# Optimization experiments

Measured on AMD Instinct MI355X. Metric: run time of the kernel, lower is better.

## Reference

```python
import jax, jax.numpy as jnp
import numpy as np

IN_DIM = 256
QK_DIM = IN_DIM // 8  # 32
B, H, W = 4, 64, 64


def setup_inputs() -> dict:
    key = jax.random.key(0)
    ks = jax.random.split(key, 8)
    s = 1.0 / np.sqrt(IN_DIM)
    return {
        "x": jax.random.normal(ks[0], (B, IN_DIM, H, W), dtype=jnp.float32),
        "Wq": jax.random.normal(ks[1], (QK_DIM, IN_DIM), dtype=jnp.float32) * s,
        "bq": jax.random.normal(ks[2], (QK_DIM,), dtype=jnp.float32) * 0.01,
        "Wk": jax.random.normal(ks[3], (QK_DIM, IN_DIM), dtype=jnp.float32) * s,
        "bk": jax.random.normal(ks[4], (QK_DIM,), dtype=jnp.float32) * 0.01,
        "Wv": jax.random.normal(ks[5], (IN_DIM, IN_DIM), dtype=jnp.float32) * s,
        "bv": jax.random.normal(ks[6], (IN_DIM,), dtype=jnp.float32) * 0.01,
        "gamma": jax.random.normal(ks[7], (1,), dtype=jnp.float32) * 0.1,
    }


def reference(x, Wq, bq, Wk, bk, Wv, bv, gamma):
    b, c, h, w = x.shape
    n = h * w
    xf = x.reshape(b, c, n)  # [b, c, n]
    # 1x1 convs are channel-wise linear maps over flattened spatial dim
    q = jnp.einsum('dc,bcn->bnd', Wq, xf) + bq  # [b, n, d]
    k = jnp.einsum('dc,bcn->bdn', Wk, xf) + bk[:, None]  # [b, d, n]
    attn = jax.nn.softmax(jnp.einsum('bnd,bdm->bnm', q, k), axis=-1)  # [b, n, n]
    v = jnp.einsum('ec,bcn->ben', Wv, xf) + bv[:, None]  # [b, c, n]
    # out[:, :, m] = sum_n v[:, :, n] * attn[m, n]  (bmm with attn^T)
    out = jnp.einsum('ben,bmn->bem', v, attn).reshape(b, c, h, w)
    return gamma * out + x
```

## Files before the change

### kernel.cpp

```cpp
#include <hip/hip_runtime.h>
#include <hip/hip_bf16.h>
#include <stdint.h>

#define DI __device__ __forceinline__

typedef float f32x4 __attribute__((ext_vector_type(4)));
typedef short bf16x8 __attribute__((ext_vector_type(8)));
typedef unsigned short u16x4 __attribute__((ext_vector_type(4)));

constexpr int BATCH = 4;
constexpr int C = 256;
constexpr int N = 4096;
constexpr int NO = 320;
constexpr int KB2 = 64;
constexpr int NT2 = N / KB2;

DI unsigned short f2bf(float f) {
  union { float f; unsigned int i; } v; v.f = f;
  unsigned int r = v.i + 0x7fffu + ((v.i >> 16) & 1u);
  return (unsigned short)(r >> 16);
}

__global__ __launch_bounds__(256) void prep_kernel(
    const float* __restrict__ Wq, const float* __restrict__ Wk, const float* __restrict__ Wv,
    const float* __restrict__ bq, const float* __restrict__ bk, const float* __restrict__ bv,
    unsigned short* __restrict__ Wcat, float* __restrict__ bcat) {
  int idx = blockIdx.x * 256 + threadIdx.x;
  if (idx < NO * C) {
    int row = idx >> 8, c = idx & 255;
    float v = (row < 32) ? Wq[row * 256 + c]
            : (row < 64) ? Wk[(row - 32) * 256 + c]
                         : Wv[(row - 64) * 256 + c];
    Wcat[idx] = f2bf(v);
  }
  if (idx < NO) {
    float v = (idx < 32) ? bq[idx] : (idx < 64) ? bk[idx - 32] : bv[idx - 64];
    bcat[idx] = v;
  }
}

__global__ __launch_bounds__(256) void proj_kernel(
    const float* __restrict__ x, const unsigned short* __restrict__ Wcat,
    const float* __restrict__ bcat,
    unsigned short* __restrict__ qarr, unsigned short* __restrict__ karr,
    unsigned short* __restrict__ vT) {
  __shared__ __align__(16) unsigned short ldsx[C][68];

  int b = blockIdx.y, n0 = blockIdx.x * 64;
  int t = threadIdx.x, lane = t & 63, w = t >> 6;
  int g = lane >> 4, cq = lane & 15;

  const float* xb = x + (size_t)b * C * N;
  {
    int csub = lane >> 4, m = lane & 15;
    #pragma unroll 4
    for (int cc = 0; cc < 16; ++cc) {
      int c = cc * 16 + w * 4 + csub;
      f32x4 v = *(const f32x4*)(xb + (size_t)c * N + n0 + m * 4);
      u16x4 h;
      h[0] = f2bf(v[0]); h[1] = f2bf(v[1]); h[2] = f2bf(v[2]); h[3] = f2bf(v[3]);
      *(u16x4*)(&ldsx[c][m * 4]) = h;
    }
  }
  __syncthreads();

  bf16x8 afrag[8];
  int nrow = w * 16 + cq;
  #pragma unroll
  for (int ks = 0; ks < 8; ++ks) {
    bf16x8 a;
    #pragma unroll
    for (int j = 0; j < 8; ++j) a[j] = (short)ldsx[ks * 32 + g * 8 + j][nrow];
    afrag[ks] = a;
  }
  __syncthreads();

  unsigned short (*vlds)[258] = (unsigned short (*)[258]) & ldsx[0][0];

  #pragma unroll 2
  for (int oc = 0; oc < 20; ++oc) {
    int o = oc * 16 + cq;
    f32x4 acc = {0.f, 0.f, 0.f, 0.f};
    const unsigned short* wrow = Wcat + o * 256;
    #pragma unroll
    for (int ks = 0; ks < 8; ++ks) {
      bf16x8 bf = *(const bf16x8*)(wrow + ks * 32 + g * 8);
      acc = __builtin_amdgcn_mfma_f32_16x16x32_bf16(afrag[ks], bf, acc, 0, 0, 0);
    }
    float bias = bcat[o];
    if (oc < 4) {
      unsigned short* dst = (oc < 2) ? qarr : karr;
      int od = ((oc & 1) << 4) + cq;
      #pragma unroll
      for (int r = 0; r < 4; ++r) {
        int n = n0 + w * 16 + g * 4 + r;
        dst[((size_t)b * N + n) * 32 + od] = f2bf(acc[r] + bias);
      }
    } else {
      int e = (oc - 4) * 16 + cq;
      #pragma unroll
      for (int r = 0; r < 4; ++r)
        vlds[w * 16 + g * 4 + r][e] = f2bf(acc[r] + bias);
    }
  }
  __syncthreads();

  #pragma unroll 4
  for (int ep = 0; ep < 64; ++ep) {
    int e = ep * 4 + w;
    vT[((size_t)b * 256 + e) * N + n0 + lane] = vlds[lane][e];
  }
}

__global__ __launch_bounds__(512) void attn_kernel(
    const unsigned short* __restrict__ qarr, const unsigned short* __restrict__ karr,
    const unsigned short* __restrict__ vT, const float* __restrict__ x,
    const float* __restrict__ gamma_p, float* __restrict__ out) {
  __shared__ __align__(16) unsigned short plds[2][2][64][40];
  __shared__ float lsc[64];

  int wg = blockIdx.x;
  int xcd = wg & 7;
  int b = xcd >> 1;
  int tile = ((wg >> 3) << 1) | (xcd & 1);

  int t = threadIdx.x, lane = t & 63, w = t >> 6;
  int g = lane >> 4, cq = lane & 15;
  int qw = w & 3, kh = w >> 2;

  const unsigned short* kb = karr + (size_t)b * N * 32;
  const unsigned short* vTb = vT + (size_t)b * C * N;

  bf16x8 qf = *(const bf16x8*)(qarr + ((size_t)b * N + tile * 64 + qw * 16 + cq) * 32 + g * 8);

  short onev = (cq == 0) ? (short)0x3F80 : (short)0;
  bf16x8 onesA = {onev, onev, onev, onev, onev, onev, onev, onev};

  f32x4 o[2][4];
  #pragma unroll
  for (int i = 0; i < 2; ++i)
    #pragma unroll
    for (int j = 0; j < 4; ++j) o[i][j] = f32x4{0.f, 0.f, 0.f, 0.f};
  f32x4 oL = {0.f, 0.f, 0.f, 0.f};

  const unsigned short* vbase = vTb + (size_t)(w * 32 + cq) * N + g * 8;
  const unsigned short* kbase = kb + (size_t)(kh * 32 + cq) * 32 + g * 8;

  bf16x8 kf0 = *(const bf16x8*)(kbase);
  bf16x8 kf1 = *(const bf16x8*)(kbase + 16 * 32);
  bf16x8 vf00 = *(const bf16x8*)(vbase);
  bf16x8 vf01 = *(const bf16x8*)(vbase + 32);
  bf16x8 vf10 = *(const bf16x8*)(vbase + 16 * N);
  bf16x8 vf11 = *(const bf16x8*)(vbase + 16 * N + 32);

  for (int nt = 0; nt < NT2; ++nt) {
    int pb = nt & 1;
    int nn2 = ((nt + 1) & (NT2 - 1)) * KB2;

    bf16x8 nk0 = *(const bf16x8*)(kbase + (size_t)nn2 * 32);
    bf16x8 nk1 = *(const bf16x8*)(kbase + (size_t)(nn2 + 16) * 32);
    bf16x8 nv00 = *(const bf16x8*)(vbase + nn2);
    bf16x8 nv01 = *(const bf16x8*)(vbase + nn2 + 32);
    bf16x8 nv10 = *(const bf16x8*)(vbase + 16 * N + nn2);
    bf16x8 nv11 = *(const bf16x8*)(vbase + 16 * N + nn2 + 32);

    f32x4 s0 = __builtin_amdgcn_mfma_f32_16x16x32_bf16(qf, kf0, f32x4{0.f,0.f,0.f,0.f}, 0, 0, 0);
    f32x4 s1 = __builtin_amdgcn_mfma_f32_16x16x32_bf16(qf, kf1, f32x4{0.f,0.f,0.f,0.f}, 0, 0, 0);

    #pragma unroll
    for (int r = 0; r < 4; ++r) {
      float p0 = __expf(s0[r] - 20.0f);
      float p1 = __expf(s1[r] - 20.0f);
      plds[pb][kh][qw * 16 + g * 4 + r][cq] = f2bf(p0);
      plds[pb][kh][qw * 16 + g * 4 + r][16 + cq] = f2bf(p1);
    }

    asm volatile("s_waitcnt lgkmcnt(0)\n\ts_barrier" ::: "memory");

    __builtin_amdgcn_s_setprio(1);
    #pragma unroll
    for (int qc = 0; qc < 4; ++qc) {
      bf16x8 pf0 = *(const bf16x8*)(&plds[pb][0][qc * 16 + cq][g * 8]);
      bf16x8 pf1 = *(const bf16x8*)(&plds[pb][1][qc * 16 + cq][g * 8]);
      o[0][qc] = __builtin_amdgcn_mfma_f32_16x16x32_bf16(vf00, pf0, o[0][qc], 0, 0, 0);
      o[0][qc] = __builtin_amdgcn_mfma_f32_16x16x32_bf16(vf01, pf1, o[0][qc], 0, 0, 0);
      o[1][qc] = __builtin_amdgcn_mfma_f32_16x16x32_bf16(vf10, pf0, o[1][qc], 0, 0, 0);
      o[1][qc] = __builtin_amdgcn_mfma_f32_16x16x32_bf16(vf11, pf1, o[1][qc], 0, 0, 0);
      if (qc == w) {
        oL = __builtin_amdgcn_mfma_f32_16x16x32_bf16(onesA, pf0, oL, 0, 0, 0);
        oL = __builtin_amdgcn_mfma_f32_16x16x32_bf16(onesA, pf1, oL, 0, 0, 0);
      }
    }
    __builtin_amdgcn_s_setprio(0);

    kf0 = nk0; kf1 = nk1;
    vf00 = nv00; vf01 = nv01; vf10 = nv10; vf11 = nv11;
  }

  if (w < 4 && lane < 16) lsc[w * 16 + lane] = gamma_p[0] / oL[0];
  __syncthreads();

  const float* xb = x + (size_t)b * C * N;
  float* ob = out + (size_t)b * C * N;
  #pragma unroll
  for (int qc = 0; qc < 4; ++qc) {
    float scale = lsc[qc * 16 + cq];
    int qg = tile * 64 + qc * 16 + cq;
    #pragma unroll
    for (int ec = 0; ec < 2; ++ec) {
      #pragma unroll
      for (int r = 0; r < 4; ++r) {
        int e = w * 32 + ec * 16 + g * 4 + r;
        size_t idx = (size_t)e * N + qg;
        ob[idx] = o[ec][qc][r] * scale + xb[idx];
      }
    }
  }
}

extern "C" void kernel_launch(void* const* d_in, const int* in_sizes, int n_in,
                              void* d_out, int out_size, void* d_ws, size_t ws_size,
                              hipStream_t stream) {
  const float* x  = (const float*)d_in[0];
  const float* Wq = (const float*)d_in[1];
  const float* bq = (const float*)d_in[2];
  const float* Wk = (const float*)d_in[3];
  const float* bk = (const float*)d_in[4];
  const float* Wv = (const float*)d_in[5];
  const float* bv = (const float*)d_in[6];
  const float* gamma = (const float*)d_in[7];
  float* out = (float*)d_out;

  char* ws = (char*)d_ws;
  unsigned short* Wcat = (unsigned short*)(ws);
  float* bcat          = (float*)(ws + 163840);
  unsigned short* qarr = (unsigned short*)(ws + 165120);
  unsigned short* karr = (unsigned short*)(ws + 1213696);
  unsigned short* vT   = (unsigned short*)(ws + 2262272);

  prep_kernel<<<320, 256, 0, stream>>>(Wq, Wk, Wv, bq, bk, bv, Wcat, bcat);
  proj_kernel<<<dim3(64, 4), 256, 0, stream>>>(x, Wcat, bcat, qarr, karr, vT);
  attn_kernel<<<256, 512, 0, stream>>>(qarr, karr, vT, x, gamma, out);
}
```

Baseline: 184.9 us.

## Split attention and projection work across more blocks, use exp2 and packed bf16 converts

The attention kernel now launches twice as many workgroups, and each one handles half of the value channels (128), which halves per-wave accumulators and V loads. Each block still recomputes the full QK scores and softmax for its query tile. The projection kernel is split along a new z grid dimension into five output-channel groups. Each group reloads and converts the x tile, so more parallel blocks are traded for redundant x reads. Q is prescaled by log2(e) so the raw v_exp_f32 can replace __expf, and packed v_cvt_pk_bf16_f32 writes combine two P values per LDS store, with keys interleaved to match.

After: 225.5 us. 1.22x slower.

```diff
diff --git a/kernel.cpp b/kernel.cpp
--- a/kernel.cpp
+++ b/kernel.cpp
@@ -6,7 +6,6 @@
 
 typedef float f32x4 __attribute__((ext_vector_type(4)));
 typedef short bf16x8 __attribute__((ext_vector_type(8)));
-typedef unsigned short u16x4 __attribute__((ext_vector_type(4)));
 
 constexpr int BATCH = 4;
 constexpr int C = 256;
@@ -14,11 +13,22 @@
 constexpr int NO = 320;
 constexpr int KB2 = 64;
 constexpr int NT2 = N / KB2;
+constexpr float LOG2E = 1.44269504088896340736f;
 
 DI unsigned short f2bf(float f) {
   union { float f; unsigned int i; } v; v.f = f;
   unsigned int r = v.i + 0x7fffu + ((v.i >> 16) & 1u);
   return (unsigned short)(r >> 16);
+}
+
+DI float exp2i(float x) {
+  float r; asm("v_exp_f32 %0, %1" : "=v"(r) : "v"(x)); return r;
+}
+
+DI unsigned int cvtpk(float lo, float hi) {
+  unsigned int r;
+  asm("v_cvt_pk_bf16_f32 %0, %1, %2" : "=v"(r) : "v"(lo), "v"(hi));
+  return r;
 }
 
 __global__ __launch_bounds__(256) void prep_kernel(
@@ -28,13 +38,14 @@
   int idx = blockIdx.x * 256 + threadIdx.x;
   if (idx < NO * C) {
     int row = idx >> 8, c = idx & 255;
-    float v = (row < 32) ? Wq[row * 256 + c]
+    float v = (row < 32) ? Wq[row * 256 + c] * LOG2E
             : (row < 64) ? Wk[(row - 32) * 256 + c]
                          : Wv[(row - 64) * 256 + c];
     Wcat[idx] = f2bf(v);
   }
   if (idx < NO) {
-    float v = (idx < 32) ? bq[idx] : (idx < 64) ? bk[idx - 32] : bv[idx - 64];
+    float v = (idx < 32) ? bq[idx] * LOG2E
+            : (idx < 64) ? bk[idx - 32] : bv[idx - 64];
     bcat[idx] = v;
   }
 }
@@ -44,9 +55,9 @@
     const float* __restrict__ bcat,
     unsigned short* __restrict__ qarr, unsigned short* __restrict__ karr,
     unsigned short* __restrict__ vT) {
-  __shared__ __align__(16) unsigned short ldsx[C][68];
-
-  int b = blockIdx.y, n0 = blockIdx.x * 64;
+  __shared__ __align__(16) unsigned short ldsx[C][66];
+
+  int b = blockIdx.y, n0 = blockIdx.x * 64, z = blockIdx.z;
   int t = threadIdx.x, lane = t & 63, w = t >> 6;
   int g = lane >> 4, cq = lane & 15;
 
@@ -57,9 +68,10 @@
     for (int cc = 0; cc < 16; ++cc) {
       int c = cc * 16 + w * 4 + csub;
       f32x4 v = *(const f32x4*)(xb + (size_t)c * N + n0 + m * 4);
-      u16x4 h;
-      h[0] = f2bf(v[0]); h[1] = f2bf(v[1]); h[2] = f2bf(v[2]); h[3] = f2bf(v[3]);
-      *(u16x4*)(&ldsx[c][m * 4]) = h;
+      unsigned int p01 = ((unsigned int)f2bf(v[0])) | ((unsigned int)f2bf(v[1]) << 16);
+      unsigned int p23 = ((unsigned int)f2bf(v[2])) | ((unsigned int)f2bf(v[3]) << 16);
+      *(unsigned int*)(&ldsx[c][m * 4]) = p01;
+      *(unsigned int*)(&ldsx[c][m * 4 + 2]) = p23;
     }
   }
   __syncthreads();
@@ -75,10 +87,11 @@
   }
   __syncthreads();
 
-  unsigned short (*vlds)[258] = (unsigned short (*)[258]) & ldsx[0][0];
-
-  #pragma unroll 2
-  for (int oc = 0; oc < 20; ++oc) {
+  unsigned short (*vlds)[66] = (unsigned short (*)[66]) & ldsx[0][0];
+
+  #pragma unroll
+  for (int i = 0; i < 4; ++i) {
+    int oc = z * 4 + i;
     int o = oc * 16 + cq;
     f32x4 acc = {0.f, 0.f, 0.f, 0.f};
     const unsigned short* wrow = Wcat + o * 256;
@@ -88,7 +101,7 @@
       acc = __builtin_amdgcn_mfma_f32_16x16x32_bf16(afrag[ks], bf, acc, 0, 0, 0);
     }
     float bias = bcat[o];
-    if (oc < 4) {
+    if (z == 0) {
       unsigned short* dst = (oc < 2) ? qarr : karr;
       int od = ((oc & 1) << 4) + cq;
       #pragma unroll
@@ -97,18 +110,21 @@
         dst[((size_t)b * N + n) * 32 + od] = f2bf(acc[r] + bias);
       }
     } else {
-      int e = (oc - 4) * 16 + cq;
+      int el = i * 16 + cq;
       #pragma unroll
       for (int r = 0; r < 4; ++r)
-        vlds[w * 16 + g * 4 + r][e] = f2bf(acc[r] + bias);
-    }
-  }
-  __syncthreads();
-
-  #pragma unroll 4
-  for (int ep = 0; ep < 64; ++ep) {
-    int e = ep * 4 + w;
-    vT[((size_t)b * 256 + e) * N + n0 + lane] = vlds[lane][e];
+        vlds[w * 16 + g * 4 + r][el] = f2bf(acc[r] + bias);
+    }
+  }
+
+  if (z > 0) {
+    __syncthreads();
+    int e0 = (z - 1) * 64;
+    #pragma unroll 4
+    for (int ep = 0; ep < 16; ++ep) {
+      int el = ep * 4 + w;
+      vT[((size_t)b * 256 + e0 + el) * N + n0 + lane] = vlds[lane][el];
+    }
   }
 }
 
@@ -116,13 +132,14 @@
     const unsigned short* __restrict__ qarr, const unsigned short* __restrict__ karr,
     const unsigned short* __restrict__ vT, const float* __restrict__ x,
     const float* __restrict__ gamma_p, float* __restrict__ out) {
-  __shared__ __align__(16) unsigned short plds[2][2][64][40];
+  __shared__ __align__(16) unsigned int plds[2][64][36];
   __shared__ float lsc[64];
 
-  int wg = blockIdx.x;
-  int xcd = wg & 7;
+  int bid = blockIdx.x;
+  int xcd = bid & 7;
   int b = xcd >> 1;
-  int tile = ((wg >> 3) << 1) | (xcd & 1);
+  int eh = (bid >> 3) & 1;
+  int tile = ((bid >> 4) << 1) | (bid & 1);
 
   int t = threadIdx.x, lane = t & 63, w = t >> 6;
   int g = lane >> 4, cq = lane & 15;
@@ -136,43 +153,38 @@
   short onev = (cq == 0) ? (short)0x3F80 : (short)0;
   bf16x8 onesA = {onev, onev, onev, onev, onev, onev, onev, onev};
 
-  f32x4 o[2][4];
-  #pragma unroll
-  for (int i = 0; i < 2; ++i)
-    #pragma unroll
-    for (int j = 0; j < 4; ++j) o[i][j] = f32x4{0.f, 0.f, 0.f, 0.f};
+  f32x4 o[4];
+  #pragma unroll
+  for (int j = 0; j < 4; ++j) o[j] = f32x4{0.f, 0.f, 0.f, 0.f};
   f32x4 oL = {0.f, 0.f, 0.f, 0.f};
 
-  const unsigned short* vbase = vTb + (size_t)(w * 32 + cq) * N + g * 8;
-  const unsigned short* kbase = kb + (size_t)(kh * 32 + cq) * 32 + g * 8;
-
-  bf16x8 kf0 = *(const bf16x8*)(kbase);
-  bf16x8 kf1 = *(const bf16x8*)(kbase + 16 * 32);
-  bf16x8 vf00 = *(const bf16x8*)(vbase);
-  bf16x8 vf01 = *(const bf16x8*)(vbase + 32);
-  bf16x8 vf10 = *(const bf16x8*)(vbase + 16 * N);
-  bf16x8 vf11 = *(const bf16x8*)(vbase + 16 * N + 32);
+  const unsigned short* vbase = vTb + (size_t)(eh * 128 + w * 16 + cq) * N + g * 8;
+  const unsigned short* kbase0 = kb + (size_t)(kh * 32 + 2 * cq) * 32 + g * 8;
+
+  bf16x8 kf0 = *(const bf16x8*)(kbase0);
+  bf16x8 kf1 = *(const bf16x8*)(kbase0 + 32);
+  bf16x8 vf0 = *(const bf16x8*)(vbase);
+  bf16x8 vf1 = *(const bf16x8*)(vbase + 32);
+
+  const float C2 = 20.0f * LOG2E;
 
   for (int nt = 0; nt < NT2; ++nt) {
     int pb = nt & 1;
     int nn2 = ((nt + 1) & (NT2 - 1)) * KB2;
 
-    bf16x8 nk0 = *(const bf16x8*)(kbase + (size_t)nn2 * 32);
-    bf16x8 nk1 = *(const bf16x8*)(kbase + (size_t)(nn2 + 16) * 32);
-    bf16x8 nv00 = *(const bf16x8*)(vbase + nn2);
-    bf16x8 nv01 = *(const bf16x8*)(vbase + nn2 + 32);
-    bf16x8 nv10 = *(const bf16x8*)(vbase + 16 * N + nn2);
-    bf16x8 nv11 = *(const bf16x8*)(vbase + 16 * N + nn2 + 32);
+    bf16x8 nk0 = *(const bf16x8*)(kbase0 + (size_t)nn2 * 32);
+    bf16x8 nk1 = *(const bf16x8*)(kbase0 + (size_t)nn2 * 32 + 32);
+    bf16x8 nv0 = *(const bf16x8*)(vbase + nn2);
+    bf16x8 nv1 = *(const bf16x8*)(vbase + nn2 + 32);
 
     f32x4 s0 = __builtin_amdgcn_mfma_f32_16x16x32_bf16(qf, kf0, f32x4{0.f,0.f,0.f,0.f}, 0, 0, 0);
     f32x4 s1 = __builtin_amdgcn_mfma_f32_16x16x32_bf16(qf, kf1, f32x4{0.f,0.f,0.f,0.f}, 0, 0, 0);
 
     #pragma unroll
     for (int r = 0; r < 4; ++r) {
-      float p0 = __expf(s0[r] - 20.0f);
-      float p1 = __expf(s1[r] - 20.0f);
-      plds[pb][kh][qw * 16 + g * 4 + r][cq] = f2bf(p0);
-      plds[pb][kh][qw * 16 + g * 4 + r][16 + cq] = f2bf(p1);
+      float p0 = exp2i(s0[r] - C2);
+      float p1 = exp2i(s1[r] - C2);
+      plds[pb][qw * 16 + g * 4 + r][kh * 16 + cq] = cvtpk(p0, p1);
     }
 
     asm volatile("s_waitcnt lgkmcnt(0)\n\ts_barrier" ::: "memory");
@@ -180,12 +192,11 @@
     __builtin_amdgcn_s_setprio(1);
     #pragma unroll
     for (int qc = 0; qc < 4; ++qc) {
-      bf16x8 pf0 = *(const bf16x8*)(&plds[pb][0][qc * 16 + cq][g * 8]);
-      bf16x8 pf1 = *(const bf16x8*)(&plds[pb][1][qc * 16 + cq][g * 8]);
-      o[0][qc] = __builtin_amdgcn_mfma_f32_16x16x32_bf16(vf00, pf0, o[0][qc], 0, 0, 0);
-      o[0][qc] = __builtin_amdgcn_mfma_f32_16x16x32_bf16(vf01, pf1, o[0][qc], 0, 0, 0);
-      o[1][qc] = __builtin_amdgcn_mfma_f32_16x16x32_bf16(vf10, pf0, o[1][qc], 0, 0, 0);
-      o[1][qc] = __builtin_amdgcn_mfma_f32_16x16x32_bf16(vf11, pf1, o[1][qc], 0, 0, 0);
+      const unsigned short* prow = (const unsigned short*)&plds[pb][qc * 16 + cq][0];
+      bf16x8 pf0 = *(const bf16x8*)(prow + g * 8);
+      bf16x8 pf1 = *(const bf16x8*)(prow + 32 + g * 8);
+      o[qc] = __builtin_amdgcn_mfma_f32_16x16x32_bf16(vf0, pf0, o[qc], 0, 0, 0);
+      o[qc] = __builtin_amdgcn_mfma_f32_16x16x32_bf16(vf1, pf1, o[qc], 0, 0, 0);
       if (qc == w) {
         oL = __builtin_amdgcn_mfma_f32_16x16x32_bf16(onesA, pf0, oL, 0, 0, 0);
         oL = __builtin_amdgcn_mfma_f32_16x16x32_bf16(onesA, pf1, oL, 0, 0, 0);
@@ -193,8 +204,7 @@
     }
     __builtin_amdgcn_s_setprio(0);
 
-    kf0 = nk0; kf1 = nk1;
-    vf00 = nv00; vf01 = nv01; vf10 = nv10; vf11 = nv11;
+    kf0 = nk0; kf1 = nk1; vf0 = nv0; vf1 = nv1;
   }
 
   if (w < 4 && lane < 16) lsc[w * 16 + lane] = gamma_p[0] / oL[0];
@@ -207,13 +217,10 @@
     float scale = lsc[qc * 16 + cq];
     int qg = tile * 64 + qc * 16 + cq;
     #pragma unroll
-    for (int ec = 0; ec < 2; ++ec) {
-      #pragma unroll
-      for (int r = 0; r < 4; ++r) {
-        int e = w * 32 + ec * 16 + g * 4 + r;
-        size_t idx = (size_t)e * N + qg;
-        ob[idx] = o[ec][qc][r] * scale + xb[idx];
-      }
+    for (int r = 0; r < 4; ++r) {
+      int e = eh * 128 + w * 16 + g * 4 + r;
+      size_t idx = (size_t)e * N + qg;
+      ob[idx] = o[qc][r] * scale + xb[idx];
     }
   }
 }
@@ -239,6 +246,6 @@
   unsigned short* vT   = (unsigned short*)(ws + 2262272);
 
   prep_kernel<<<320, 256, 0, stream>>>(Wq, Wk, Wv, bq, bk, bv, Wcat, bcat);
-  proj_kernel<<<dim3(64, 4), 256, 0, stream>>>(x, Wcat, bcat, qarr, karr, vT);
-  attn_kernel<<<256, 512, 0, stream>>>(qarr, karr, vT, x, gamma, out);
-}
+  proj_kernel<<<dim3(64, 4, 5), 256, 0, stream>>>(x, Wcat, bcat, qarr, karr, vT);
+  attn_kernel<<<512, 512, 0, stream>>>(qarr, karr, vT, x, gamma, out);
+}
```
